# Kernel tuning notes

Hardware: AMD Instinct MI355X
Metric: run time of the kernel (lower is better)

The kernel has to match this reference:

```python
import jax, jax.numpy as jnp
import numpy as np

B, N_ELEM, N_NODES, E2 = 4096, 2048, 1024, 4096


def setup_inputs() -> dict:
    key = jax.random.key(0)
    k = jax.random.split(key, 7)
    return {
        "EA": jax.random.normal(k[0], (B, N_ELEM), dtype=jnp.float32),
        "e": jax.random.normal(k[1], (B, N_ELEM), dtype=jnp.float32),
        "q": jax.random.normal(k[2], (B, N_NODES, 2), dtype=jnp.float32),
        "r": jax.random.normal(k[3], (B, N_NODES, 2), dtype=jnp.float32),
        "vecs": jax.random.normal(k[4], (E2, 2), dtype=jnp.float32),
        "node_ids": jax.random.randint(k[5], (E2,), 0, N_NODES, dtype=jnp.int32),
        "elem_ids": jax.random.randint(k[6], (E2,), 0, N_ELEM, dtype=jnp.int32),
    }


def reference(EA, e, q, r, vecs, node_ids, elem_ids):
    # axial_forces = EA * e : [B, N_ELEM]
    axial = EA * e
    # gather per incidence entry and scale by the 2-vector: [B, E2, 2]
    contrib = axial[:, elem_ids][..., None] * vecs[None, :, :]
    n_sample, n_nodes = q.shape[0], q.shape[1]
    # scatter-add contributions into per-node residual: [B, N_NODES, 2]
    residual = jnp.zeros((n_sample, n_nodes, 2), dtype=EA.dtype)
    residual = residual.at[:, node_ids, :].add(contrib)
    residual = residual - q - r
    return jnp.mean(jnp.square(residual))
```

## Files before the change

kernel.cpp:

```cpp
#include <hip/hip_runtime.h>

#define B_SAMPLES 4096
#define N_ELEM    2048
#define N_NODES   1024
#define E2        4096
#define BLOCK     256
#define MBLOCK    512
#define SLOTS     32
#define S         4
#define MAIN_BLOCKS (B_SAMPLES / S)

#define WS_CNT_OFF   0
#define WS_ELL_OFF   4096
#define WS_PART_OFF  (4096 + SLOTS * N_NODES * 16)

__global__ __launch_bounds__(BLOCK) void neq_zero_kernel(
    float4* __restrict__ ell, int* __restrict__ cnt)
{
    const int i = blockIdx.x * BLOCK + threadIdx.x;
    ell[i] = make_float4(0.f, 0.f, 0.f, 0.f);
    if (i < N_NODES) cnt[i] = 0;
}

__global__ __launch_bounds__(BLOCK) void neq_build_kernel(
    const float* __restrict__ vecs, const int* __restrict__ node_ids,
    const int* __restrict__ elem_ids, int* __restrict__ cnt,
    float4* __restrict__ ell)
{
    const int j = blockIdx.x * BLOCK + threadIdx.x;
    int nid = node_ids[j];
    int eid = elem_ids[j];
    float2 v = ((const float2*)vecs)[j];
    int slot = atomicAdd(&cnt[nid], 1);
    if (slot < SLOTS) {
        ell[slot * N_NODES + nid] = make_float4(v.x, v.y, __int_as_float(eid), 0.f);
    }
}

#define FMA4(A, V, W) do { (A).x += (V).x * (W); (A).y += (V).y * (W); \
                           (A).z += (V).z * (W); (A).w += (V).w * (W); } while (0)

__global__ __launch_bounds__(MBLOCK, 4) void neq_main_kernel(
    const float* __restrict__ EA, const float* __restrict__ e,
    const float* __restrict__ q,  const float* __restrict__ r,
    const int* __restrict__ cnt, const float4* __restrict__ ell,
    float* __restrict__ partial)
{
    __shared__ float4 axial4[N_ELEM];
    __shared__ float red[MBLOCK / 64];

    const int b0 = blockIdx.x * S;
    const int t = threadIdx.x;

#pragma unroll
    for (int i = 0; i < N_ELEM / MBLOCK; ++i) {
        int eid = t + i * MBLOCK;
        float4 p;
        const float* EAp = EA + (size_t)b0 * N_ELEM + eid;
        const float* ep  = e  + (size_t)b0 * N_ELEM + eid;
        p.x = EAp[0 * N_ELEM] * ep[0 * N_ELEM];
        p.y = EAp[1 * N_ELEM] * ep[1 * N_ELEM];
        p.z = EAp[2 * N_ELEM] * ep[2 * N_ELEM];
        p.w = EAp[3 * N_ELEM] * ep[3 * N_ELEM];
        axial4[eid] = p;
    }

    int c0n = min(cnt[t], SLOTS);
    int c1n = min(cnt[t + MBLOCK], SLOTS);
    int kmax = max(c0n, c1n);
    __syncthreads();

    float4 accx0 = make_float4(0.f, 0.f, 0.f, 0.f);
    float4 accy0 = make_float4(0.f, 0.f, 0.f, 0.f);
    float4 accx1 = make_float4(0.f, 0.f, 0.f, 0.f);
    float4 accy1 = make_float4(0.f, 0.f, 0.f, 0.f);

    float4 c00 = ell[t];
    float4 c01 = ell[t + MBLOCK];
    float4 c10 = ell[N_NODES + t];
    float4 c11 = ell[N_NODES + t + MBLOCK];

    for (int k0 = 0; k0 < kmax; k0 += 2) {
        int kp = k0 + 2;
        if (kp > SLOTS - 2) kp = SLOTS - 2;
        const float4* nrow = ell + (size_t)kp * N_NODES;
        float4 n00 = nrow[t];
        float4 n01 = nrow[t + MBLOCK];
        float4 n10 = nrow[N_NODES + t];
        float4 n11 = nrow[N_NODES + t + MBLOCK];

        float4 ax00 = axial4[__float_as_int(c00.z)];
        float4 ax01 = axial4[__float_as_int(c01.z)];
        float4 ax10 = axial4[__float_as_int(c10.z)];
        float4 ax11 = axial4[__float_as_int(c11.z)];
        FMA4(accx0, ax00, c00.x);  FMA4(accy0, ax00, c00.y);
        FMA4(accx1, ax01, c01.x);  FMA4(accy1, ax01, c01.y);
        FMA4(accx0, ax10, c10.x);  FMA4(accy0, ax10, c10.y);
        FMA4(accx1, ax11, c11.x);  FMA4(accy1, ax11, c11.y);

        c00 = n00; c01 = n01; c10 = n10; c11 = n11;
    }

    float acc = 0.f;
#pragma unroll
    for (int s = 0; s < S; ++s) {
        const float2* q2 = (const float2*)(q + (size_t)(b0 + s) * N_NODES * 2);
        const float2* r2 = (const float2*)(r + (size_t)(b0 + s) * N_NODES * 2);
        float2 qa = q2[t];
        float2 ra = r2[t];
        float2 qb = q2[t + MBLOCK];
        float2 rb = r2[t + MBLOCK];
        float ax0 = (s == 0) ? accx0.x : (s == 1) ? accx0.y : (s == 2) ? accx0.z : accx0.w;
        float ay0 = (s == 0) ? accy0.x : (s == 1) ? accy0.y : (s == 2) ? accy0.z : accy0.w;
        float ax1 = (s == 0) ? accx1.x : (s == 1) ? accx1.y : (s == 2) ? accx1.z : accx1.w;
        float ay1 = (s == 0) ? accy1.x : (s == 1) ? accy1.y : (s == 2) ? accy1.z : accy1.w;
        float x = ax0 - qa.x - ra.x;
        float y = ay0 - qa.y - ra.y;
        acc += x * x + y * y;
        x = ax1 - qb.x - rb.x;
        y = ay1 - qb.y - rb.y;
        acc += x * x + y * y;
    }

#pragma unroll
    for (int off = 32; off > 0; off >>= 1)
        acc += __shfl_down(acc, off, 64);
    if ((t & 63) == 0) red[t >> 6] = acc;
    __syncthreads();
    if (t == 0) {
        float s = 0.f;
#pragma unroll
        for (int w = 0; w < MBLOCK / 64; ++w) s += red[w];
        partial[blockIdx.x] = s;
    }
}

__global__ __launch_bounds__(1024) void neq_reduce_kernel(
    const float* __restrict__ partial, float* __restrict__ out)
{
    __shared__ float red[1024 / 64];
    const int t = threadIdx.x;
    float acc = partial[t];
#pragma unroll
    for (int off = 32; off > 0; off >>= 1)
        acc += __shfl_down(acc, off, 64);
    if ((t & 63) == 0) red[t >> 6] = acc;
    __syncthreads();
    if (t == 0) {
        float s = 0.f;
#pragma unroll
        for (int w = 0; w < 1024 / 64; ++w) s += red[w];
        const float inv_n = 1.0f / (float)((size_t)B_SAMPLES * N_NODES * 2);
        out[0] = s * inv_n;
    }
}

extern "C" void kernel_launch(void* const* d_in, const int* in_sizes, int n_in,
                              void* d_out, int out_size, void* d_ws, size_t ws_size,
                              hipStream_t stream) {
    const float* EA       = (const float*)d_in[0];
    const float* e        = (const float*)d_in[1];
    const float* q        = (const float*)d_in[2];
    const float* r        = (const float*)d_in[3];
    const float* vecs     = (const float*)d_in[4];
    const int*   node_ids = (const int*)d_in[5];
    const int*   elem_ids = (const int*)d_in[6];

    char* ws = (char*)d_ws;
    int*    cnt     = (int*)(ws + WS_CNT_OFF);
    float4* ell     = (float4*)(ws + WS_ELL_OFF);
    float*  partial = (float*)(ws + WS_PART_OFF);

    neq_zero_kernel<<<(SLOTS * N_NODES) / BLOCK, BLOCK, 0, stream>>>(ell, cnt);
    neq_build_kernel<<<E2 / BLOCK, BLOCK, 0, stream>>>(
        vecs, node_ids, elem_ids, cnt, ell);
    neq_main_kernel<<<MAIN_BLOCKS, MBLOCK, 0, stream>>>(
        EA, e, q, r, cnt, ell, partial);
    neq_reduce_kernel<<<1, 1024, 0, stream>>>(partial, (float*)d_out);
}
```

Baseline: 161.6 us.

## Precompute interleaved axial forces in separate kernel fused with workspace zeroing

```diff
diff --git a/kernel.cpp b/kernel.cpp
--- a/kernel.cpp
+++ b/kernel.cpp
@@ -8,11 +8,45 @@
 #define MBLOCK    512
 #define SLOTS     32
 #define S         4
-#define MAIN_BLOCKS (B_SAMPLES / S)
+#define NGROUP    (B_SAMPLES / S)
+#define AX_ELEMS  ((size_t)NGROUP * N_ELEM)
 
 #define WS_CNT_OFF   0
-#define WS_ELL_OFF   4096
-#define WS_PART_OFF  (4096 + SLOTS * N_NODES * 16)
+#define WS_PART_OFF  4096
+#define WS_ELL_OFF   8192
+#define WS_AX_OFF    (8192 + SLOTS * N_NODES * 16)
+#define WS_NEEDED    ((size_t)WS_AX_OFF + AX_ELEMS * 16)
+
+__global__ __launch_bounds__(BLOCK) void neq_axial_kernel(
+    const float* __restrict__ EA, const float* __restrict__ e,
+    float4* __restrict__ ax, float4* __restrict__ ell, int* __restrict__ cnt)
+{
+    const int blk = blockIdx.x;
+    const int t = threadIdx.x;
+
+    {
+        int i = blk * BLOCK + t;
+        if (i < SLOTS * N_NODES) ell[i] = make_float4(0.f, 0.f, 0.f, 0.f);
+        if (i < N_NODES) cnt[i] = 0;
+    }
+
+    const int g = blk >> 1;
+    const int ebase = (blk & 1) * 1024;
+    const int b0 = g * S;
+    const float* EAb = EA + (size_t)b0 * N_ELEM + ebase;
+    const float* eb  = e  + (size_t)b0 * N_ELEM + ebase;
+    float4* outb = ax + (size_t)g * N_ELEM + ebase;
+
+#pragma unroll
+    for (int i = 0; i < 4; ++i) {
+        const int eoff = t + i * BLOCK;
+        float p0 = EAb[0 * N_ELEM + eoff] * eb[0 * N_ELEM + eoff];
+        float p1 = EAb[1 * N_ELEM + eoff] * eb[1 * N_ELEM + eoff];
+        float p2 = EAb[2 * N_ELEM + eoff] * eb[2 * N_ELEM + eoff];
+        float p3 = EAb[3 * N_ELEM + eoff] * eb[3 * N_ELEM + eoff];
+        outb[eoff] = make_float4(p0, p1, p2, p3);
+    }
+}
 
 __global__ __launch_bounds__(BLOCK) void neq_zero_kernel(
     float4* __restrict__ ell, int* __restrict__ cnt)
@@ -41,7 +75,7 @@
                            (A).z += (V).z * (W); (A).w += (V).w * (W); } while (0)
 
 __global__ __launch_bounds__(MBLOCK, 4) void neq_main_kernel(
-    const float* __restrict__ EA, const float* __restrict__ e,
+    const float4* __restrict__ ax,
     const float* __restrict__ q,  const float* __restrict__ r,
     const int* __restrict__ cnt, const float4* __restrict__ ell,
     float* __restrict__ partial)
@@ -49,25 +83,24 @@
     __shared__ float4 axial4[N_ELEM];
     __shared__ float red[MBLOCK / 64];
 
-    const int b0 = blockIdx.x * S;
-    const int t = threadIdx.x;
-
-#pragma unroll
-    for (int i = 0; i < N_ELEM / MBLOCK; ++i) {
-        int eid = t + i * MBLOCK;
-        float4 p;
-        const float* EAp = EA + (size_t)b0 * N_ELEM + eid;
-        const float* ep  = e  + (size_t)b0 * N_ELEM + eid;
-        p.x = EAp[0 * N_ELEM] * ep[0 * N_ELEM];
-        p.y = EAp[1 * N_ELEM] * ep[1 * N_ELEM];
-        p.z = EAp[2 * N_ELEM] * ep[2 * N_ELEM];
-        p.w = EAp[3 * N_ELEM] * ep[3 * N_ELEM];
-        axial4[eid] = p;
-    }
+    const int g = blockIdx.x;
+    const int b0 = g * S;
+    const int t = threadIdx.x;
+
+    const float4* src = ax + (size_t)g * N_ELEM;
+    float4 s0 = src[t];
+    float4 s1 = src[t + 512];
+    float4 s2 = src[t + 1024];
+    float4 s3 = src[t + 1536];
 
     int c0n = min(cnt[t], SLOTS);
     int c1n = min(cnt[t + MBLOCK], SLOTS);
     int kmax = max(c0n, c1n);
+
+    axial4[t]        = s0;
+    axial4[t + 512]  = s1;
+    axial4[t + 1024] = s2;
+    axial4[t + 1536] = s3;
     __syncthreads();
 
     float4 accx0 = make_float4(0.f, 0.f, 0.f, 0.f);
@@ -75,30 +108,20 @@
     float4 accx1 = make_float4(0.f, 0.f, 0.f, 0.f);
     float4 accy1 = make_float4(0.f, 0.f, 0.f, 0.f);
 
-    float4 c00 = ell[t];
-    float4 c01 = ell[t + MBLOCK];
-    float4 c10 = ell[N_NODES + t];
-    float4 c11 = ell[N_NODES + t + MBLOCK];
-
     for (int k0 = 0; k0 < kmax; k0 += 2) {
-        int kp = k0 + 2;
-        if (kp > SLOTS - 2) kp = SLOTS - 2;
-        const float4* nrow = ell + (size_t)kp * N_NODES;
-        float4 n00 = nrow[t];
-        float4 n01 = nrow[t + MBLOCK];
-        float4 n10 = nrow[N_NODES + t];
-        float4 n11 = nrow[N_NODES + t + MBLOCK];
-
-        float4 ax00 = axial4[__float_as_int(c00.z)];
-        float4 ax01 = axial4[__float_as_int(c01.z)];
-        float4 ax10 = axial4[__float_as_int(c10.z)];
-        float4 ax11 = axial4[__float_as_int(c11.z)];
-        FMA4(accx0, ax00, c00.x);  FMA4(accy0, ax00, c00.y);
-        FMA4(accx1, ax01, c01.x);  FMA4(accy1, ax01, c01.y);
-        FMA4(accx0, ax10, c10.x);  FMA4(accy0, ax10, c10.y);
-        FMA4(accx1, ax11, c11.x);  FMA4(accy1, ax11, c11.y);
-
-        c00 = n00; c01 = n01; c10 = n10; c11 = n11;
+        const float4* row = ell + (size_t)k0 * N_NODES;
+        float4 pk00 = row[t];
+        float4 pk01 = row[t + MBLOCK];
+        float4 pk10 = row[N_NODES + t];
+        float4 pk11 = row[N_NODES + t + MBLOCK];
+        float4 ax00 = axial4[__float_as_int(pk00.z)];
+        float4 ax01 = axial4[__float_as_int(pk01.z)];
+        float4 ax10 = axial4[__float_as_int(pk10.z)];
+        float4 ax11 = axial4[__float_as_int(pk11.z)];
+        FMA4(accx0, ax00, pk00.x);  FMA4(accy0, ax00, pk00.y);
+        FMA4(accx1, ax01, pk01.x);  FMA4(accy1, ax01, pk01.y);
+        FMA4(accx0, ax10, pk10.x);  FMA4(accy0, ax10, pk10.y);
+        FMA4(accx1, ax11, pk11.x);  FMA4(accy1, ax11, pk11.y);
     }
 
     float acc = 0.f;
@@ -135,6 +158,90 @@
     }
 }
 
+__global__ __launch_bounds__(MBLOCK, 4) void neq_main_fallback(
+    const float* __restrict__ EA, const float* __restrict__ e,
+    const float* __restrict__ q,  const float* __restrict__ r,
+    const int* __restrict__ cnt, const float4* __restrict__ ell,
+    float* __restrict__ partial)
+{
+    __shared__ float4 axial4[N_ELEM];
+    __shared__ float red[MBLOCK / 64];
+
+    const int b0 = blockIdx.x * S;
+    const int t = threadIdx.x;
+
+#pragma unroll
+    for (int i = 0; i < N_ELEM / MBLOCK; ++i) {
+        int eid = t + i * MBLOCK;
+        float4 p;
+        const float* EAp = EA + (size_t)b0 * N_ELEM + eid;
+        const float* ep  = e  + (size_t)b0 * N_ELEM + eid;
+        p.x = EAp[0 * N_ELEM] * ep[0 * N_ELEM];
+        p.y = EAp[1 * N_ELEM] * ep[1 * N_ELEM];
+        p.z = EAp[2 * N_ELEM] * ep[2 * N_ELEM];
+        p.w = EAp[3 * N_ELEM] * ep[3 * N_ELEM];
+        axial4[eid] = p;
+    }
+    int c0n = min(cnt[t], SLOTS);
+    int c1n = min(cnt[t + MBLOCK], SLOTS);
+    int kmax = max(c0n, c1n);
+    __syncthreads();
+
+    float4 accx0 = make_float4(0.f, 0.f, 0.f, 0.f);
+    float4 accy0 = make_float4(0.f, 0.f, 0.f, 0.f);
+    float4 accx1 = make_float4(0.f, 0.f, 0.f, 0.f);
+    float4 accy1 = make_float4(0.f, 0.f, 0.f, 0.f);
+
+    for (int k0 = 0; k0 < kmax; k0 += 2) {
+        const float4* row = ell + (size_t)k0 * N_NODES;
+        float4 pk00 = row[t];
+        float4 pk01 = row[t + MBLOCK];
+        float4 pk10 = row[N_NODES + t];
+        float4 pk11 = row[N_NODES + t + MBLOCK];
+        float4 ax00 = axial4[__float_as_int(pk00.z)];
+        float4 ax01 = axial4[__float_as_int(pk01.z)];
+        float4 ax10 = axial4[__float_as_int(pk10.z)];
+        float4 ax11 = axial4[__float_as_int(pk11.z)];
+        FMA4(accx0, ax00, pk00.x);  FMA4(accy0, ax00, pk00.y);
+        FMA4(accx1, ax01, pk01.x);  FMA4(accy1, ax01, pk01.y);
+        FMA4(accx0, ax10, pk10.x);  FMA4(accy0, ax10, pk10.y);
+        FMA4(accx1, ax11, pk11.x);  FMA4(accy1, ax11, pk11.y);
+    }
+
+    float acc = 0.f;
+#pragma unroll
+    for (int s = 0; s < S; ++s) {
+        const float2* q2 = (const float2*)(q + (size_t)(b0 + s) * N_NODES * 2);
+        const float2* r2 = (const float2*)(r + (size_t)(b0 + s) * N_NODES * 2);
+        float2 qa = q2[t];
+        float2 ra = r2[t];
+        float2 qb = q2[t + MBLOCK];
+        float2 rb = r2[t + MBLOCK];
+        float ax0 = (s == 0) ? accx0.x : (s == 1) ? accx0.y : (s == 2) ? accx0.z : accx0.w;
+        float ay0 = (s == 0) ? accy0.x : (s == 1) ? accy0.y : (s == 2) ? accy0.z : accy0.w;
+        float ax1 = (s == 0) ? accx1.x : (s == 1) ? accx1.y : (s == 2) ? accx1.z : accx1.w;
+        float ay1 = (s == 0) ? accy1.x : (s == 1) ? accy1.y : (s == 2) ? accy1.z : accy1.w;
+        float x = ax0 - qa.x - ra.x;
+        float y = ay0 - qa.y - ra.y;
+        acc += x * x + y * y;
+        x = ax1 - qb.x - rb.x;
+        y = ay1 - qb.y - rb.y;
+        acc += x * x + y * y;
+    }
+
+#pragma unroll
+    for (int off = 32; off > 0; off >>= 1)
+        acc += __shfl_down(acc, off, 64);
+    if ((t & 63) == 0) red[t >> 6] = acc;
+    __syncthreads();
+    if (t == 0) {
+        float s = 0.f;
+#pragma unroll
+        for (int w = 0; w < MBLOCK / 64; ++w) s += red[w];
+        partial[blockIdx.x] = s;
+    }
+}
+
 __global__ __launch_bounds__(1024) void neq_reduce_kernel(
     const float* __restrict__ partial, float* __restrict__ out)
 {
@@ -168,13 +275,22 @@
 
     char* ws = (char*)d_ws;
     int*    cnt     = (int*)(ws + WS_CNT_OFF);
+    float*  partial = (float*)(ws + WS_PART_OFF);
     float4* ell     = (float4*)(ws + WS_ELL_OFF);
-    float*  partial = (float*)(ws + WS_PART_OFF);
-
-    neq_zero_kernel<<<(SLOTS * N_NODES) / BLOCK, BLOCK, 0, stream>>>(ell, cnt);
-    neq_build_kernel<<<E2 / BLOCK, BLOCK, 0, stream>>>(
-        vecs, node_ids, elem_ids, cnt, ell);
-    neq_main_kernel<<<MAIN_BLOCKS, MBLOCK, 0, stream>>>(
-        EA, e, q, r, cnt, ell, partial);
+    float4* ax      = (float4*)(ws + WS_AX_OFF);
+
+    if (ws_size >= WS_NEEDED) {
+        neq_axial_kernel<<<2 * NGROUP, BLOCK, 0, stream>>>(EA, e, ax, ell, cnt);
+        neq_build_kernel<<<E2 / BLOCK, BLOCK, 0, stream>>>(
+            vecs, node_ids, elem_ids, cnt, ell);
+        neq_main_kernel<<<NGROUP, MBLOCK, 0, stream>>>(
+            ax, q, r, cnt, ell, partial);
+    } else {
+        neq_zero_kernel<<<(SLOTS * N_NODES) / BLOCK, BLOCK, 0, stream>>>(ell, cnt);
+        neq_build_kernel<<<E2 / BLOCK, BLOCK, 0, stream>>>(
+            vecs, node_ids, elem_ids, cnt, ell);
+        neq_main_fallback<<<NGROUP, MBLOCK, 0, stream>>>(
+            EA, e, q, r, cnt, ell, partial);
+    }
     neq_reduce_kernel<<<1, 1024, 0, stream>>>(partial, (float*)d_out);
 }
```

Result: slower. 172.3 us (+6.6%).
